# Kernel tuning notes

Measured on AMD Instinct MI355X. Metric: run time of the kernel, lower is better.

Reference implementation:

```python
import jax, jax.numpy as jnp
import numpy as np

N_NODES = 100000
N_EDGES = 1600000
IN_DIM, HID_DIM, OUT_DIM = 128, 128, 64


def setup_inputs() -> dict:
    key = jax.random.key(0)
    k1, k2, k3, k4, k5 = jax.random.split(key, 5)
    x = jax.random.normal(k1, (N_NODES, IN_DIM), dtype=jnp.float32)
    edge_index = jax.random.randint(k2, (2, N_EDGES), 0, N_NODES, dtype=jnp.int64)
    # PyG GCNConv linear weights (no bias); Glorot-ish scale for stability
    W1 = jax.random.normal(k3, (IN_DIM, HID_DIM), dtype=jnp.float32) * 0.05
    W2 = jax.random.normal(k4, (HID_DIM, HID_DIM), dtype=jnp.float32) * 0.05
    W3 = jax.random.normal(k5, (HID_DIM, OUT_DIM), dtype=jnp.float32) * 0.05
    return {"x": x, "edge_index": edge_index, "W1": W1, "W2": W2, "W3": W3}


def _gcn_conv(h, W, src, dst, num_nodes):
    # GCNConv(add_self_loops=False, normalize=False, bias=False):
    # linear transform, then scatter-add messages from src into dst
    msg = jnp.take(h @ W, src, axis=0)          # [E, d_out] gather
    return jax.ops.segment_sum(msg, dst, num_segments=num_nodes)  # [N, d_out]


def reference(x, edge_index, W1, W2, W3):
    num_nodes = x.shape[0]
    src, dst = edge_index[0], edge_index[1]
    h = jax.nn.relu(_gcn_conv(x, W1, src, dst, num_nodes))
    # dropout p=0.0 / eval mode -> identity
    h = jax.nn.relu(_gcn_conv(h, W2, src, dst, num_nodes))
    out = _gcn_conv(h, W3, src, dst, num_nodes)
    return jax.nn.log_softmax(out, axis=1)
```

## Files before the change

### kernel.cpp

```cpp
#include <hip/hip_runtime.h>
#include <hip/hip_bf16.h>

#define KDIM 128

typedef __attribute__((ext_vector_type(8))) __bf16 bf16x8;
typedef __attribute__((ext_vector_type(4))) float f32x4;
typedef __attribute__((ext_vector_type(2))) float f32x2;

static __device__ __forceinline__ unsigned short f2bf(float f) {
  unsigned u = __float_as_uint(f);
  u += 0x7fffu + ((u >> 16) & 1u);
  return (unsigned short)(u >> 16);
}
static __device__ __forceinline__ unsigned pack_bf16x2(float a, float b) {
  return (unsigned)f2bf(a) | ((unsigned)f2bf(b) << 16);
}
static __device__ __forceinline__ float2 unpack_bf16x2(unsigned u) {
  return make_float2(__uint_as_float(u << 16), __uint_as_float(u & 0xffff0000u));
}
static __device__ __forceinline__ unsigned relu2(unsigned u) {
  unsigned r = u;
  if (u & 0x00008000u) r &= 0xffff0000u;
  if (u & 0x80000000u) r &= 0x0000ffffu;
  return r;
}

static __device__ __forceinline__ unsigned char f2fp8(float f) {
#if __has_builtin(__builtin_amdgcn_cvt_pk_fp8_f32)
  return (unsigned char)(__builtin_amdgcn_cvt_pk_fp8_f32(f, f, 0, false) & 0xff);
#else
  unsigned s = (__float_as_uint(f) >> 24) & 0x80u;
  float a = fminf(fabsf(f), 448.f);
  if (a < 0.015625f) {
    unsigned m = (unsigned)(a * 512.f + 0.5f);
    return (unsigned char)(s | m);
  }
  unsigned v = __float_as_uint(a);
  v += 0x7ffffu + ((v >> 20) & 1u);
  unsigned em = (v >> 20) - 960u;
  if (em > 0x7eu) em = 0x7eu;
  return (unsigned char)(s | em);
#endif
}
static __device__ __forceinline__ float fp8dec(unsigned b) {
  unsigned s = (b & 0x80u) << 24;
  unsigned em = b & 0x7fu;
  float mag = (em >= 8) ? __uint_as_float((em + 960u) << 20)
                        : (float)em * 0.001953125f;
  return __uint_as_float(__float_as_uint(mag) | s);
}
static __device__ __forceinline__ float4 fp8x4_to_f32(unsigned u) {
#if __has_builtin(__builtin_amdgcn_cvt_pk_f32_fp8)
  f32x2 lo = __builtin_amdgcn_cvt_pk_f32_fp8(u, false);
  f32x2 hi = __builtin_amdgcn_cvt_pk_f32_fp8(u, true);
  return make_float4(lo[0], lo[1], hi[0], hi[1]);
#else
  return make_float4(fp8dec(u & 255u), fp8dec((u >> 8) & 255u),
                     fp8dec((u >> 16) & 255u), fp8dec(u >> 24));
#endif
}

__global__ __launch_bounds__(256) void wtrans_k(const float* __restrict__ W,
                                                unsigned short* __restrict__ Wt,
                                                int NOUT) {
  const int t = blockIdx.x * 256 + threadIdx.x;
  if (t >= NOUT * KDIM) return;
  const int n = t >> 7;
  const int k = t & 127;
  Wt[t] = f2bf(W[k * NOUT + n]);
}

template<int NOUT, bool AF32, bool RELU>
__global__ __launch_bounds__(512) void gemm_mfma_k(const void* __restrict__ Av,
                                                   const unsigned short* __restrict__ Wt,
                                                   unsigned char* __restrict__ C, int M) {
  constexpr int NT = NOUT / 16;
  __shared__ unsigned short Ws[NOUT][136];

  const int tid = threadIdx.x;
  for (int i = tid; i < NOUT * 16; i += 512) {
    const int n = i >> 4, k8 = i & 15;
    const uint4 v = *reinterpret_cast<const uint4*>(&Wt[n * KDIM + k8 * 8]);
    *reinterpret_cast<uint4*>(&Ws[n][k8 * 8]) = v;
  }

  const int wv = tid >> 6;
  const int l  = tid & 63;
  const int am = l & 15;
  const int kb = l >> 4;
  const int arow_g = blockIdx.x * 128 + wv * 16 + am;
  const bool valid = arow_g < M;
  const int arow = valid ? arow_g : 0;

  uint4 afr[4];
  if constexpr (AF32) {
    const float* A = (const float*)Av;
    #pragma unroll
    for (int ks = 0; ks < 4; ++ks) {
      const float4 lo = *reinterpret_cast<const float4*>(&A[(size_t)arow * 128 + ks * 32 + kb * 8]);
      const float4 hi = *reinterpret_cast<const float4*>(&A[(size_t)arow * 128 + ks * 32 + kb * 8 + 4]);
      afr[ks] = make_uint4(pack_bf16x2(lo.x, lo.y), pack_bf16x2(lo.z, lo.w),
                           pack_bf16x2(hi.x, hi.y), pack_bf16x2(hi.z, hi.w));
    }
  } else {
    const unsigned* A = (const unsigned*)Av;
    #pragma unroll
    for (int ks = 0; ks < 4; ++ks) {
      uint4 u = *reinterpret_cast<const uint4*>(&A[(size_t)arow * 64 + ks * 16 + kb * 4]);
      if constexpr (RELU) {
        u.x = relu2(u.x); u.y = relu2(u.y); u.z = relu2(u.z); u.w = relu2(u.w);
      }
      afr[ks] = u;
    }
  }
  if (!valid) {
    afr[0] = make_uint4(0, 0, 0, 0); afr[1] = afr[0];
    afr[2] = afr[0];                 afr[3] = afr[0];
  }

  f32x4 acc[NT];
  #pragma unroll
  for (int nt = 0; nt < NT; ++nt) {
    acc[nt][0] = 0.f; acc[nt][1] = 0.f; acc[nt][2] = 0.f; acc[nt][3] = 0.f;
  }

  __syncthreads();
  #pragma unroll
  for (int ks = 0; ks < 4; ++ks) {
    const bf16x8 a = __builtin_bit_cast(bf16x8, afr[ks]);
    #pragma unroll
    for (int nt = 0; nt < NT; ++nt) {
      const uint4 bv = *reinterpret_cast<const uint4*>(&Ws[nt * 16 + am][ks * 32 + kb * 8]);
      acc[nt] = __builtin_amdgcn_mfma_f32_16x16x32_bf16(
          a, __builtin_bit_cast(bf16x8, bv), acc[nt], 0, 0, 0);
    }
  }

  const int crow0 = blockIdx.x * 128 + wv * 16 + kb * 4;
  #pragma unroll
  for (int nt = 0; nt < NT; ++nt) {
    #pragma unroll
    for (int r = 0; r < 4; ++r) {
      const int rr = crow0 + r;
      if (rr < M) C[(size_t)rr * NOUT + nt * 16 + am] = f2fp8(acc[nt][r]);
    }
  }
}

__global__ __launch_bounds__(512) void hist_k(const int* __restrict__ dst,
                                              int* __restrict__ histT, int E) {
  __shared__ int h[256];
  if (threadIdx.x < 256) h[threadIdx.x] = 0;
  __syncthreads();
  const int E4 = E >> 2;
  for (int i = blockIdx.x * 512 + threadIdx.x; i < E4; i += 256 * 512) {
    const int4 d4 = *reinterpret_cast<const int4*>(&dst[i * 4]);
    atomicAdd(&h[d4.x >> 9], 1);
    atomicAdd(&h[d4.y >> 9], 1);
    atomicAdd(&h[d4.z >> 9], 1);
    atomicAdd(&h[d4.w >> 9], 1);
  }
  if (blockIdx.x == 0 && threadIdx.x < (E & 3))
    atomicAdd(&h[dst[E4 * 4 + threadIdx.x] >> 9], 1);
  __syncthreads();
  if (threadIdx.x < 256) histT[threadIdx.x * 256 + blockIdx.x] = h[threadIdx.x];
}

__global__ __launch_bounds__(256) void scan1_k(const int* __restrict__ in,
                                               int* __restrict__ out,
                                               int* __restrict__ bsum, int N) {
  __shared__ int ls[256];
  const int t = threadIdx.x;
  const int base = blockIdx.x * 2048 + t * 8;
  int v[8];
  if (base + 8 <= N) {
    *reinterpret_cast<int4*>(&v[0]) = *reinterpret_cast<const int4*>(&in[base]);
    *reinterpret_cast<int4*>(&v[4]) = *reinterpret_cast<const int4*>(&in[base + 4]);
  } else {
    #pragma unroll
    for (int j = 0; j < 8; ++j) v[j] = (base + j < N) ? in[base + j] : 0;
  }
  int s = 0;
  #pragma unroll
  for (int j = 0; j < 8; ++j) { const int tmp = v[j]; v[j] = s; s += tmp; }
  int x = s;
  ls[t] = x;
  __syncthreads();
  for (int off = 1; off < 256; off <<= 1) {
    int y = 0;
    if (t >= off) y = ls[t - off];
    __syncthreads();
    x += y;
    ls[t] = x;
    __syncthreads();
  }
  const int excl = x - s;
  #pragma unroll
  for (int j = 0; j < 8; ++j)
    if (base + j < N) out[base + j] = excl + v[j];
  if (t == 255) bsum[blockIdx.x] = x;
}

__global__ __launch_bounds__(64) void scan2_k(const int* __restrict__ bsum,
                                              int* __restrict__ bscan, int NB) {
  const int t = threadIdx.x;
  const int v = (t < NB) ? bsum[t] : 0;
  int x = v;
  #pragma unroll
  for (int off = 1; off < 64; off <<= 1) {
    const int y = __shfl_up(x, off, 64);
    if (t >= off) x += y;
  }
  bscan[t] = x - v;
}

__global__ __launch_bounds__(256) void addoff_k(int* __restrict__ off,
                                                const int* __restrict__ bscan) {
  const int i = blockIdx.x * 256 + threadIdx.x;
  off[i] += bscan[i >> 11];
}

__global__ __launch_bounds__(512) void binscatter_k(const int* __restrict__ src,
                                                    const int* __restrict__ dst,
                                                    const int* __restrict__ histOff,
                                                    unsigned* __restrict__ epack,
                                                    int E) {
  __shared__ int cur[256];
  if (threadIdx.x < 256) cur[threadIdx.x] = histOff[threadIdx.x * 256 + blockIdx.x];
  __syncthreads();
  const int E4 = E >> 2;
  for (int i = blockIdx.x * 512 + threadIdx.x; i < E4; i += 256 * 512) {
    const int4 d4 = *reinterpret_cast<const int4*>(&dst[i * 4]);
    const int4 s4 = *reinterpret_cast<const int4*>(&src[i * 4]);
    int p;
    p = atomicAdd(&cur[d4.x >> 9], 1); epack[p] = ((unsigned)(d4.x & 511) << 17) | (unsigned)s4.x;
    p = atomicAdd(&cur[d4.y >> 9], 1); epack[p] = ((unsigned)(d4.y & 511) << 17) | (unsigned)s4.y;
    p = atomicAdd(&cur[d4.z >> 9], 1); epack[p] = ((unsigned)(d4.z & 511) << 17) | (unsigned)s4.z;
    p = atomicAdd(&cur[d4.w >> 9], 1); epack[p] = ((unsigned)(d4.w & 511) << 17) | (unsigned)s4.w;
  }
  if (blockIdx.x == 0 && threadIdx.x < (E & 3)) {
    const int e = E4 * 4 + threadIdx.x;
    const int d = dst[e];
    const int p = atomicAdd(&cur[d >> 9], 1);
    epack[p] = ((unsigned)(d & 511) << 17) | (unsigned)src[e];
  }
}

__global__ __launch_bounds__(512) void binsort_k(const unsigned* __restrict__ epack,
                                                 const int* __restrict__ histOff,
                                                 int* __restrict__ rowptr,
                                                 int* __restrict__ col,
                                                 int N, int E) {
  __shared__ int hist[512];
  __shared__ int ls[256];
  __shared__ int cur[512];
  const int b = blockIdx.x;
  const int t = threadIdx.x;
  const int nbins = (N + 511) >> 9;
  const int beg = histOff[b * 256];
  const int end = (b + 1 < nbins) ? histOff[(b + 1) * 256] : E;

  hist[t] = 0;
  __syncthreads();
  for (int j = beg + t; j < end; j += 512)
    atomicAdd(&hist[epack[j] >> 17], 1);
  __syncthreads();

  int a = 0, b2 = 0, x = 0;
  if (t < 256) { a = hist[2 * t]; b2 = hist[2 * t + 1]; x = a + b2; ls[t] = x; }
  __syncthreads();
  for (int off = 1; off < 256; off <<= 1) {
    int y = 0;
    if (t < 256 && t >= off) y = ls[t - off];
    __syncthreads();
    if (t < 256) { x += y; ls[t] = x; }
    __syncthreads();
  }
  if (t < 256) {
    const int excl = x - a - b2;
    cur[2 * t] = excl;
    cur[2 * t + 1] = excl + a;
    const int g0 = b * 512 + 2 * t;
    if (g0 <= N) rowptr[g0] = beg + excl;
    if (g0 + 1 <= N) rowptr[g0 + 1] = beg + excl + a;
  }
  __syncthreads();
  for (int j = beg + t; j < end; j += 512) {
    const unsigned p = epack[j];
    const int pos = atomicAdd(&cur[p >> 17], 1);
    col[beg + pos] = (int)(p & 0x1ffffu);
  }
}

__global__ __launch_bounds__(256) void gather128_k(const unsigned* __restrict__ H32,
                                                   const int* __restrict__ rowptr,
                                                   const int* __restrict__ col,
                                                   unsigned* __restrict__ out, int N) {
  const int w = (int)((blockIdx.x * 256u + threadIdx.x) >> 6);
  const int lane = threadIdx.x & 63;
  const int h = lane >> 5;
  const int l5 = lane & 31;
  if (w >= N) return;
  const int beg = __builtin_amdgcn_readfirstlane(rowptr[w]);
  const int end = __builtin_amdgcn_readfirstlane(rowptr[w + 1]);

  float4 acc0 = make_float4(0.f, 0.f, 0.f, 0.f);
  float4 acc1 = make_float4(0.f, 0.f, 0.f, 0.f);
  float4 acc2 = make_float4(0.f, 0.f, 0.f, 0.f);
  float4 acc3 = make_float4(0.f, 0.f, 0.f, 0.f);

  int e = beg;
  for (; e + 16 <= end; e += 16) {
    const int s0 = col[e + h];
    const int s1 = col[e + 2 + h];
    const int s2 = col[e + 4 + h];
    const int s3 = col[e + 6 + h];
    const int s4 = col[e + 8 + h];
    const int s5 = col[e + 10 + h];
    const int s6 = col[e + 12 + h];
    const int s7 = col[e + 14 + h];
    const unsigned u0 = H32[(size_t)s0 * 32 + l5];
    const unsigned u1 = H32[(size_t)s1 * 32 + l5];
    const unsigned u2 = H32[(size_t)s2 * 32 + l5];
    const unsigned u3 = H32[(size_t)s3 * 32 + l5];
    const unsigned u4 = H32[(size_t)s4 * 32 + l5];
    const unsigned u5 = H32[(size_t)s5 * 32 + l5];
    const unsigned u6 = H32[(size_t)s6 * 32 + l5];
    const unsigned u7 = H32[(size_t)s7 * 32 + l5];
    float4 v;
    v = fp8x4_to_f32(u0); acc0.x += v.x; acc0.y += v.y; acc0.z += v.z; acc0.w += v.w;
    v = fp8x4_to_f32(u1); acc1.x += v.x; acc1.y += v.y; acc1.z += v.z; acc1.w += v.w;
    v = fp8x4_to_f32(u2); acc2.x += v.x; acc2.y += v.y; acc2.z += v.z; acc2.w += v.w;
    v = fp8x4_to_f32(u3); acc3.x += v.x; acc3.y += v.y; acc3.z += v.z; acc3.w += v.w;
    v = fp8x4_to_f32(u4); acc0.x += v.x; acc0.y += v.y; acc0.z += v.z; acc0.w += v.w;
    v = fp8x4_to_f32(u5); acc1.x += v.x; acc1.y += v.y; acc1.z += v.z; acc1.w += v.w;
    v = fp8x4_to_f32(u6); acc2.x += v.x; acc2.y += v.y; acc2.z += v.z; acc2.w += v.w;
    v = fp8x4_to_f32(u7); acc3.x += v.x; acc3.y += v.y; acc3.z += v.z; acc3.w += v.w;
  }
  for (; e + 8 <= end; e += 8) {
    const int s0 = col[e + h];
    const int s1 = col[e + 2 + h];
    const int s2 = col[e + 4 + h];
    const int s3 = col[e + 6 + h];
    const unsigned u0 = H32[(size_t)s0 * 32 + l5];
    const unsigned u1 = H32[(size_t)s1 * 32 + l5];
    const unsigned u2 = H32[(size_t)s2 * 32 + l5];
    const unsigned u3 = H32[(size_t)s3 * 32 + l5];
    float4 v;
    v = fp8x4_to_f32(u0); acc0.x += v.x; acc0.y += v.y; acc0.z += v.z; acc0.w += v.w;
    v = fp8x4_to_f32(u1); acc1.x += v.x; acc1.y += v.y; acc1.z += v.z; acc1.w += v.w;
    v = fp8x4_to_f32(u2); acc2.x += v.x; acc2.y += v.y; acc2.z += v.z; acc2.w += v.w;
    v = fp8x4_to_f32(u3); acc3.x += v.x; acc3.y += v.y; acc3.z += v.z; acc3.w += v.w;
  }
  for (; e + 2 <= end; e += 2) {
    const float4 v = fp8x4_to_f32(H32[(size_t)col[e + h] * 32 + l5]);
    acc0.x += v.x; acc0.y += v.y; acc0.z += v.z; acc0.w += v.w;
  }
  if (e < end && h == 0) {
    const float4 v = fp8x4_to_f32(H32[(size_t)col[e] * 32 + l5]);
    acc1.x += v.x; acc1.y += v.y; acc1.z += v.z; acc1.w += v.w;
  }

  float4 a;
  a.x = (acc0.x + acc1.x) + (acc2.x + acc3.x);
  a.y = (acc0.y + acc1.y) + (acc2.y + acc3.y);
  a.z = (acc0.z + acc1.z) + (acc2.z + acc3.z);
  a.w = (acc0.w + acc1.w) + (acc2.w + acc3.w);
  a.x += __shfl_xor(a.x, 32, 64);
  a.y += __shfl_xor(a.y, 32, 64);
  a.z += __shfl_xor(a.z, 32, 64);
  a.w += __shfl_xor(a.w, 32, 64);

  if (h == 0) {
    *reinterpret_cast<uint2*>(&out[(size_t)w * 64 + l5 * 2]) =
        make_uint2(pack_bf16x2(a.x, a.y), pack_bf16x2(a.z, a.w));
  }
}

__global__ __launch_bounds__(256) void gather64lsm_k(const unsigned* __restrict__ H32,
                                                     const int* __restrict__ rowptr,
                                                     const int* __restrict__ col,
                                                     float* __restrict__ out, int N) {
  const int w = (int)((blockIdx.x * 256u + threadIdx.x) >> 6);
  const int lane = threadIdx.x & 63;
  const int q = lane >> 4;
  const int l4 = lane & 15;
  if (w >= N) return;
  const int beg = __builtin_amdgcn_readfirstlane(rowptr[w]);
  const int end = __builtin_amdgcn_readfirstlane(rowptr[w + 1]);

  float4 acc0 = make_float4(0.f, 0.f, 0.f, 0.f);
  float4 acc1 = make_float4(0.f, 0.f, 0.f, 0.f);

  int e = beg;
  for (; e + 16 <= end; e += 16) {
    const int s0 = col[e + q];
    const int s1 = col[e + 4 + q];
    const int s2 = col[e + 8 + q];
    const int s3 = col[e + 12 + q];
    const unsigned u0 = H32[(size_t)s0 * 16 + l4];
    const unsigned u1 = H32[(size_t)s1 * 16 + l4];
    const unsigned u2 = H32[(size_t)s2 * 16 + l4];
    const unsigned u3 = H32[(size_t)s3 * 16 + l4];
    float4 v;
    v = fp8x4_to_f32(u0); acc0.x += v.x; acc0.y += v.y; acc0.z += v.z; acc0.w += v.w;
    v = fp8x4_to_f32(u1); acc1.x += v.x; acc1.y += v.y; acc1.z += v.z; acc1.w += v.w;
    v = fp8x4_to_f32(u2); acc0.x += v.x; acc0.y += v.y; acc0.z += v.z; acc0.w += v.w;
    v = fp8x4_to_f32(u3); acc1.x += v.x; acc1.y += v.y; acc1.z += v.z; acc1.w += v.w;
  }
  for (; e + 8 <= end; e += 8) {
    const int s0 = col[e + q];
    const int s1 = col[e + 4 + q];
    const float4 v0 = fp8x4_to_f32(H32[(size_t)s0 * 16 + l4]);
    const float4 v1 = fp8x4_to_f32(H32[(size_t)s1 * 16 + l4]);
    acc0.x += v0.x; acc0.y += v0.y; acc0.z += v0.z; acc0.w += v0.w;
    acc1.x += v1.x; acc1.y += v1.y; acc1.z += v1.z; acc1.w += v1.w;
  }
  if (e + 4 <= end) {
    const float4 v = fp8x4_to_f32(H32[(size_t)col[e + q] * 16 + l4]);
    acc0.x += v.x; acc0.y += v.y; acc0.z += v.z; acc0.w += v.w;
    e += 4;
  }
  if (e + q < end) {
    const float4 v = fp8x4_to_f32(H32[(size_t)col[e + q] * 16 + l4]);
    acc1.x += v.x; acc1.y += v.y; acc1.z += v.z; acc1.w += v.w;
  }

  float4 a;
  a.x = acc0.x + acc1.x;
  a.y = acc0.y + acc1.y;
  a.z = acc0.z + acc1.z;
  a.w = acc0.w + acc1.w;
  a.x += __shfl_xor(a.x, 16, 64); a.x += __shfl_xor(a.x, 32, 64);
  a.y += __shfl_xor(a.y, 16, 64); a.y += __shfl_xor(a.y, 32, 64);
  a.z += __shfl_xor(a.z, 16, 64); a.z += __shfl_xor(a.z, 32, 64);
  a.w += __shfl_xor(a.w, 16, 64); a.w += __shfl_xor(a.w, 32, 64);

  float m = fmaxf(fmaxf(a.x, a.y), fmaxf(a.z, a.w));
  #pragma unroll
  for (int o = 8; o > 0; o >>= 1) m = fmaxf(m, __shfl_xor(m, o, 64));
  float s = __expf(a.x - m) + __expf(a.y - m) + __expf(a.z - m) + __expf(a.w - m);
  #pragma unroll
  for (int o = 8; o > 0; o >>= 1) s += __shfl_xor(s, o, 64);
  const float ls = __logf(s);

  if (lane < 16) {
    *reinterpret_cast<float4*>(&out[(size_t)w * 64 + l4 * 4]) =
        make_float4(a.x - m - ls, a.y - m - ls, a.z - m - ls, a.w - m - ls);
  }
}

extern "C" void kernel_launch(void* const* d_in, const int* in_sizes, int n_in,
                              void* d_out, int out_size, void* d_ws, size_t ws_size,
                              hipStream_t stream) {
  const float* x  = (const float*)d_in[0];
  const int*   ei = (const int*)d_in[1];
  const float* W1 = (const float*)d_in[2];
  const float* W2 = (const float*)d_in[3];
  const float* W3 = (const float*)d_in[4];
  float* out = (float*)d_out;

  const int N = in_sizes[0] / KDIM;
  const int E = in_sizes[1] / 2;
  const int* src = ei;
  const int* dst = ei + E;

  unsigned char* H = (unsigned char*)d_ws;
  unsigned* AGGp = (unsigned*)(H + (size_t)N * 128);
  unsigned short* Wt1 = (unsigned short*)(AGGp + (size_t)N * 64);
  unsigned short* Wt2 = Wt1 + 128 * 128;
  unsigned short* Wt3 = Wt2 + 128 * 128;
  int* col     = (int*)(Wt3 + 64 * 128);
  int* rowptr  = col + E;
  int* histT   = rowptr + (N + 8);
  int* histOff = histT + 65536;
  int* bsum2   = histOff + 65536;
  int* bscan2  = bsum2 + 64;
  unsigned* epack = (unsigned*)AGGp;

  const int nbins = (N + 511) / 512;

  wtrans_k<<<(128 * 128 + 255) / 256, 256, 0, stream>>>(W1, Wt1, 128);
  wtrans_k<<<(128 * 128 + 255) / 256, 256, 0, stream>>>(W2, Wt2, 128);
  wtrans_k<<<(64 * 128 + 255) / 256, 256, 0, stream>>>(W3, Wt3, 64);

  hist_k<<<256, 512, 0, stream>>>(dst, histT, E);
  scan1_k<<<32, 256, 0, stream>>>(histT, histOff, bsum2, 65536);
  scan2_k<<<1, 64, 0, stream>>>(bsum2, bscan2, 32);
  addoff_k<<<256, 256, 0, stream>>>(histOff, bscan2);
  binscatter_k<<<256, 512, 0, stream>>>(src, dst, histOff, epack, E);
  binsort_k<<<nbins, 512, 0, stream>>>(epack, histOff, rowptr, col, N, E);

  const int gemm_grid = (N + 127) / 128;
  const int gather_grid = (N + 3) / 4;

  gemm_mfma_k<128, true, false><<<gemm_grid, 512, 0, stream>>>(x, Wt1, H, N);
  gather128_k<<<gather_grid, 256, 0, stream>>>((const unsigned*)H, rowptr, col, AGGp, N);

  gemm_mfma_k<128, false, true><<<gemm_grid, 512, 0, stream>>>(AGGp, Wt2, H, N);
  gather128_k<<<gather_grid, 256, 0, stream>>>((const unsigned*)H, rowptr, col, AGGp, N);

  gemm_mfma_k<64, false, true><<<gemm_grid, 512, 0, stream>>>(AGGp, Wt3, H, N);
  gather64lsm_k<<<gather_grid, 256, 0, stream>>>((const unsigned*)H, rowptr, col, out, N);
}
```

Before: 221.7 us.

## Store GEMM output in column panels and gather per panel for cache locality

The 128-wide GEMM outputs are now written as four 32-byte column panels of shape [N][32] instead of row-major [N][128]. The 128-wide gather is reorganised so that each block handles one panel over half of the node range, with 8 lanes per node, and blocks are interleaved across the panel and half indices. The aim is to shrink the randomly gathered working set per panel (about 3.2 MB of fp8) so it stays in L2/MALL and random row fetches get more cache hits. It also adds nontemporal loads of col and nontemporal stores of the output. The cost is that col indices are re-read four times, once per panel, and each gathered access is only 4 bytes per lane.

```diff
diff --git a/kernel.cpp b/kernel.cpp
--- a/kernel.cpp
+++ b/kernel.cpp
@@ -70,7 +70,7 @@
   Wt[t] = f2bf(W[k * NOUT + n]);
 }
 
-template<int NOUT, bool AF32, bool RELU>
+template<int NOUT, bool AF32, bool RELU, bool PANEL>
 __global__ __launch_bounds__(512) void gemm_mfma_k(const void* __restrict__ Av,
                                                    const unsigned short* __restrict__ Wt,
                                                    unsigned char* __restrict__ C, int M) {
@@ -139,10 +139,17 @@
   const int crow0 = blockIdx.x * 128 + wv * 16 + kb * 4;
   #pragma unroll
   for (int nt = 0; nt < NT; ++nt) {
+    const int c = nt * 16 + am;
     #pragma unroll
     for (int r = 0; r < 4; ++r) {
       const int rr = crow0 + r;
-      if (rr < M) C[(size_t)rr * NOUT + nt * 16 + am] = f2fp8(acc[nt][r]);
+      if (rr < M) {
+        if constexpr (PANEL) {
+          C[(size_t)(c >> 5) * M * 32 + (size_t)rr * 32 + (c & 31)] = f2fp8(acc[nt][r]);
+        } else {
+          C[(size_t)rr * NOUT + c] = f2fp8(acc[nt][r]);
+        }
+      }
     }
   }
 }
@@ -292,89 +299,63 @@
   }
 }
 
-__global__ __launch_bounds__(256) void gather128_k(const unsigned* __restrict__ H32,
+__global__ __launch_bounds__(256) void gather128_k(const unsigned* __restrict__ Hp,
                                                    const int* __restrict__ rowptr,
                                                    const int* __restrict__ col,
-                                                   unsigned* __restrict__ out, int N) {
-  const int w = (int)((blockIdx.x * 256u + threadIdx.x) >> 6);
-  const int lane = threadIdx.x & 63;
-  const int h = lane >> 5;
-  const int l5 = lane & 31;
-  if (w >= N) return;
-  const int beg = __builtin_amdgcn_readfirstlane(rowptr[w]);
-  const int end = __builtin_amdgcn_readfirstlane(rowptr[w + 1]);
-
-  float4 acc0 = make_float4(0.f, 0.f, 0.f, 0.f);
-  float4 acc1 = make_float4(0.f, 0.f, 0.f, 0.f);
-  float4 acc2 = make_float4(0.f, 0.f, 0.f, 0.f);
-  float4 acc3 = make_float4(0.f, 0.f, 0.f, 0.f);
+                                                   unsigned* __restrict__ out,
+                                                   int N, int Nh) {
+  const int g8 = blockIdx.x & 7;
+  const int half = g8 >> 2;
+  const int grp = g8 & 3;
+  const int t = threadIdx.x;
+  const int lo = half * Nh;
+  const int hi = (lo + Nh < N) ? lo + Nh : N;
+  const int node = lo + (int)(blockIdx.x >> 3) * 32 + (t >> 3);
+  const int cl = t & 7;
+  if (node >= hi) return;
+
+  const unsigned* P = Hp + (size_t)grp * N * 8;
+  const int beg = rowptr[node];
+  const int end = rowptr[node + 1];
+
+  float4 a0 = make_float4(0.f, 0.f, 0.f, 0.f);
+  float4 a1 = make_float4(0.f, 0.f, 0.f, 0.f);
+  float4 a2 = make_float4(0.f, 0.f, 0.f, 0.f);
+  float4 a3 = make_float4(0.f, 0.f, 0.f, 0.f);
 
   int e = beg;
-  for (; e + 16 <= end; e += 16) {
-    const int s0 = col[e + h];
-    const int s1 = col[e + 2 + h];
-    const int s2 = col[e + 4 + h];
-    const int s3 = col[e + 6 + h];
-    const int s4 = col[e + 8 + h];
-    const int s5 = col[e + 10 + h];
-    const int s6 = col[e + 12 + h];
-    const int s7 = col[e + 14 + h];
-    const unsigned u0 = H32[(size_t)s0 * 32 + l5];
-    const unsigned u1 = H32[(size_t)s1 * 32 + l5];
-    const unsigned u2 = H32[(size_t)s2 * 32 + l5];
-    const unsigned u3 = H32[(size_t)s3 * 32 + l5];
-    const unsigned u4 = H32[(size_t)s4 * 32 + l5];
-    const unsigned u5 = H32[(size_t)s5 * 32 + l5];
-    const unsigned u6 = H32[(size_t)s6 * 32 + l5];
-    const unsigned u7 = H32[(size_t)s7 * 32 + l5];
+  for (; e + 4 <= end; e += 4) {
+    const int s0 = __builtin_nontemporal_load(&col[e]);
+    const int s1 = __builtin_nontemporal_load(&col[e + 1]);
+    const int s2 = __builtin_nontemporal_load(&col[e + 2]);
+    const int s3 = __builtin_nontemporal_load(&col[e + 3]);
+    const unsigned u0 = P[(size_t)s0 * 8 + cl];
+    const unsigned u1 = P[(size_t)s1 * 8 + cl];
+    const unsigned u2 = P[(size_t)s2 * 8 + cl];
+    const unsigned u3 = P[(size_t)s3 * 8 + cl];
     float4 v;
-    v = fp8x4_to_f32(u0); acc0.x += v.x; acc0.y += v.y; acc0.z += v.z; acc0.w += v.w;
-    v = fp8x4_to_f32(u1); acc1.x += v.x; acc1.y += v.y; acc1.z += v.z; acc1.w += v.w;
-    v = fp8x4_to_f32(u2); acc2.x += v.x; acc2.y += v.y; acc2.z += v.z; acc2.w += v.w;
-    v = fp8x4_to_f32(u3); acc3.x += v.x; acc3.y += v.y; acc3.z += v.z; acc3.w += v.w;
-    v = fp8x4_to_f32(u4); acc0.x += v.x; acc0.y += v.y; acc0.z += v.z; acc0.w += v.w;
-    v = fp8x4_to_f32(u5); acc1.x += v.x; acc1.y += v.y; acc1.z += v.z; acc1.w += v.w;
-    v = fp8x4_to_f32(u6); acc2.x += v.x; acc2.y += v.y; acc2.z += v.z; acc2.w += v.w;
-    v = fp8x4_to_f32(u7); acc3.x += v.x; acc3.y += v.y; acc3.z += v.z; acc3.w += v.w;
-  }
-  for (; e + 8 <= end; e += 8) {
-    const int s0 = col[e + h];
-    const int s1 = col[e + 2 + h];
-    const int s2 = col[e + 4 + h];
-    const int s3 = col[e + 6 + h];
-    const unsigned u0 = H32[(size_t)s0 * 32 + l5];
-    const unsigned u1 = H32[(size_t)s1 * 32 + l5];
-    const unsigned u2 = H32[(size_t)s2 * 32 + l5];
-    const unsigned u3 = H32[(size_t)s3 * 32 + l5];
-    float4 v;
-    v = fp8x4_to_f32(u0); acc0.x += v.x; acc0.y += v.y; acc0.z += v.z; acc0.w += v.w;
-    v = fp8x4_to_f32(u1); acc1.x += v.x; acc1.y += v.y; acc1.z += v.z; acc1.w += v.w;
-    v = fp8x4_to_f32(u2); acc2.x += v.x; acc2.y += v.y; acc2.z += v.z; acc2.w += v.w;
-    v = fp8x4_to_f32(u3); acc3.x += v.x; acc3.y += v.y; acc3.z += v.z; acc3.w += v.w;
-  }
-  for (; e + 2 <= end; e += 2) {
-    const float4 v = fp8x4_to_f32(H32[(size_t)col[e + h] * 32 + l5]);
-    acc0.x += v.x; acc0.y += v.y; acc0.z += v.z; acc0.w += v.w;
-  }
-  if (e < end && h == 0) {
-    const float4 v = fp8x4_to_f32(H32[(size_t)col[e] * 32 + l5]);
-    acc1.x += v.x; acc1.y += v.y; acc1.z += v.z; acc1.w += v.w;
+    v = fp8x4_to_f32(u0); a0.x += v.x; a0.y += v.y; a0.z += v.z; a0.w += v.w;
+    v = fp8x4_to_f32(u1); a1.x += v.x; a1.y += v.y; a1.z += v.z; a1.w += v.w;
+    v = fp8x4_to_f32(u2); a2.x += v.x; a2.y += v.y; a2.z += v.z; a2.w += v.w;
+    v = fp8x4_to_f32(u3); a3.x += v.x; a3.y += v.y; a3.z += v.z; a3.w += v.w;
+  }
+  for (; e < end; ++e) {
+    const int s = __builtin_nontemporal_load(&col[e]);
+    const float4 v = fp8x4_to_f32(P[(size_t)s * 8 + cl]);
+    a0.x += v.x; a0.y += v.y; a0.z += v.z; a0.w += v.w;
   }
 
   float4 a;
-  a.x = (acc0.x + acc1.x) + (acc2.x + acc3.x);
-  a.y = (acc0.y + acc1.y) + (acc2.y + acc3.y);
-  a.z = (acc0.z + acc1.z) + (acc2.z + acc3.z);
-  a.w = (acc0.w + acc1.w) + (acc2.w + acc3.w);
-  a.x += __shfl_xor(a.x, 32, 64);
-  a.y += __shfl_xor(a.y, 32, 64);
-  a.z += __shfl_xor(a.z, 32, 64);
-  a.w += __shfl_xor(a.w, 32, 64);
-
-  if (h == 0) {
-    *reinterpret_cast<uint2*>(&out[(size_t)w * 64 + l5 * 2]) =
-        make_uint2(pack_bf16x2(a.x, a.y), pack_bf16x2(a.z, a.w));
-  }
+  a.x = (a0.x + a1.x) + (a2.x + a3.x);
+  a.y = (a0.y + a1.y) + (a2.y + a3.y);
+  a.z = (a0.z + a1.z) + (a2.z + a3.z);
+  a.w = (a0.w + a1.w) + (a2.w + a3.w);
+
+  const unsigned long long pk =
+      (unsigned long long)pack_bf16x2(a.x, a.y) |
+      ((unsigned long long)pack_bf16x2(a.z, a.w) << 32);
+  __builtin_nontemporal_store(
+      pk, (unsigned long long*)&out[(size_t)node * 64 + grp * 16 + cl * 2]);
 }
 
 __global__ __launch_bounds__(256) void gather64lsm_k(const unsigned* __restrict__ H32,
@@ -493,13 +474,15 @@
 
   const int gemm_grid = (N + 127) / 128;
   const int gather_grid = (N + 3) / 4;
-
-  gemm_mfma_k<128, true, false><<<gemm_grid, 512, 0, stream>>>(x, Wt1, H, N);
-  gather128_k<<<gather_grid, 256, 0, stream>>>((const unsigned*)H, rowptr, col, AGGp, N);
-
-  gemm_mfma_k<128, false, true><<<gemm_grid, 512, 0, stream>>>(AGGp, Wt2, H, N);
-  gather128_k<<<gather_grid, 256, 0, stream>>>((const unsigned*)H, rowptr, col, AGGp, N);
-
-  gemm_mfma_k<64, false, true><<<gemm_grid, 512, 0, stream>>>(AGGp, Wt3, H, N);
+  const int Nh = (N + 1) / 2;
+  const int g128_grid = ((Nh + 31) / 32) * 8;
+
+  gemm_mfma_k<128, true, false, true><<<gemm_grid, 512, 0, stream>>>(x, Wt1, H, N);
+  gather128_k<<<g128_grid, 256, 0, stream>>>((const unsigned*)H, rowptr, col, AGGp, N, Nh);
+
+  gemm_mfma_k<128, false, true, true><<<gemm_grid, 512, 0, stream>>>(AGGp, Wt2, H, N);
+  gather128_k<<<g128_grid, 256, 0, stream>>>((const unsigned*)H, rowptr, col, AGGp, N, Nh);
+
+  gemm_mfma_k<64, false, true, false><<<gemm_grid, 512, 0, stream>>>(AGGp, Wt3, H, N);
   gather64lsm_k<<<gather_grid, 256, 0, stream>>>((const unsigned*)H, rowptr, col, out, N);
 }
```

Result: slower. 283.9 us (+28.1%).
